# Kernel tuning notes

Measured on AMD Instinct MI355X. Metric: run time of the kernel, lower is better.

Reference implementation:

```python
import jax, jax.numpy as jnp
import numpy as np

B, T, C = 4, 2048, 1024
N_HEAD = 16
HEAD_DIM = C // N_HEAD


def setup_inputs() -> dict:
    key = jax.random.key(0)
    k1, k2, k3 = jax.random.split(key, 3)
    scale = 0.02
    x = jax.random.normal(k1, (B, T, C), dtype=jnp.float32)
    W_attn = jax.random.normal(k2, (C, 3 * C), dtype=jnp.float32) * scale
    b_attn = jnp.zeros((3 * C,), dtype=jnp.float32)
    W_proj = jax.random.normal(k3, (C, C), dtype=jnp.float32) * scale
    b_proj = jnp.zeros((C,), dtype=jnp.float32)
    return {"x": x, "W_attn": W_attn, "b_attn": b_attn, "W_proj": W_proj, "b_proj": b_proj}


def reference(x, W_attn, b_attn, W_proj, b_proj):
    Bx, Tx, Cx = x.shape
    qkv = x @ W_attn + b_attn                      # [B,T,3C]
    q, k, v = jnp.split(qkv, 3, axis=-1)
    def split_heads(t):
        return t.reshape(Bx, Tx, N_HEAD, HEAD_DIM).transpose(0, 2, 1, 3)  # [B,H,T,D]
    q, k, v = split_heads(q), split_heads(k), split_heads(v)
    att = jnp.einsum('bhqd,bhkd->bhqk', q, k) / jnp.sqrt(jnp.float32(HEAD_DIM))
    causal = jnp.tril(jnp.ones((Tx, Tx), dtype=bool))
    att = jnp.where(causal, att, jnp.float32(-jnp.inf))
    att = jax.nn.softmax(att, axis=-1)
    y = jnp.einsum('bhqk,bhkd->bhqd', att, v)      # [B,H,T,D]
    y = y.transpose(0, 2, 1, 3).reshape(Bx, Tx, Cx)
    return y @ W_proj + b_proj
```

## Files before the change

kernel.cpp:

```cpp
#include <hip/hip_runtime.h>
#include <hip/hip_bf16.h>
#include <math.h>

#define B_  4
#define T_  2048
#define C_  1024
#define NH  16
#define HD  64
#define M_  (B_ * T_)
#define N_QKV (3 * C_)
#define KDIM 1024
#define SCALE2 0.18033688011112042f

typedef __attribute__((ext_vector_type(8))) short short8;
typedef __attribute__((ext_vector_type(4))) short bs4;
typedef __attribute__((ext_vector_type(4))) float f32x4;
typedef __attribute__((ext_vector_type(16))) float f32x16;
typedef __attribute__((ext_vector_type(4))) unsigned u32x4;

__device__ __forceinline__ short f2bs(float f) {
  __hip_bfloat16 h = __float2bfloat16(f);
  return *reinterpret_cast<short*>(&h);
}
__device__ __forceinline__ unsigned pack2(float a, float b) {
  return (unsigned)(unsigned short)f2bs(a) | ((unsigned)(unsigned short)f2bs(b) << 16);
}

__device__ __forceinline__ void gload16(const void* g, void* l) {
  __builtin_amdgcn_global_load_lds(
      (const __attribute__((address_space(1))) void*)g,
      (__attribute__((address_space(3))) void*)l, 16, 0, 0);
}

__global__ __launch_bounds__(256) void wtrans_kernel(
    const float* __restrict__ W, short* __restrict__ Wt, int Ncols, int qcols)
{
  __shared__ short t[32][33];
  const int nb = Ncols / 32;
  const int bn = blockIdx.x % nb, bk = blockIdx.x / nb;
  const int tid = threadIdx.x;
  const int r = tid >> 3, c4 = (tid & 7) * 4;
  const float cs = (bn * 32 < qcols) ? SCALE2 : 1.f;
  f32x4 v = *reinterpret_cast<const f32x4*>(
      W + (size_t)(bk * 32 + r) * Ncols + bn * 32 + c4);
  #pragma unroll
  for (int j = 0; j < 4; ++j) t[r][c4 + j] = f2bs(v[j] * cs);
  __syncthreads();
  bs4 o;
  #pragma unroll
  for (int j = 0; j < 4; ++j) o[j] = t[c4 + j][r];
  *reinterpret_cast<bs4*>(Wt + (size_t)(bn * 32 + r) * KDIM + bk * 32 + c4) = o;
}

template<bool A_BF16, bool OUT_BF16>
__global__ __launch_bounds__(256) void gemm128_kernel(
    const void* __restrict__ Aptr, const short* __restrict__ Bt,
    const float* __restrict__ bias, void* __restrict__ outptr, int N, int nq)
{
  __shared__ short As[128 * 32];
  __shared__ short Bs[128 * 32];

  const int tid  = threadIdx.x;
  const int lane = tid & 63;
  const int w    = tid >> 6;
  const int wr   = w >> 1, wc = w & 1;
  const int rl   = lane & 15, kg = lane >> 4;
  const int nblk = N >> 7;
  const int m0 = (blockIdx.x / nblk) << 7;
  const int n0 = (blockIdx.x % nblk) << 7;

  f32x4 acc[4][4] = {};

  const int srow = w * 32 + (lane >> 2);
  const int scol = ((lane & 3) ^ ((lane >> 3) & 3)) * 8;
  const short* pb0 = Bt + (size_t)(n0 + srow) * KDIM + scol;
  const short* pb1 = pb0 + (size_t)16 * KDIM;
  short* const lb0 = &Bs[w * 1024];
  short* const lb1 = &Bs[w * 1024 + 512];

  const short* pa0 = nullptr; const short* pa1 = nullptr;
  short* la0 = nullptr; short* la1 = nullptr;
  const float* paf = nullptr; short* lafA = nullptr; short* lafB = nullptr;
  if constexpr (A_BF16) {
    pa0 = (const short*)Aptr + (size_t)(m0 + srow) * KDIM + scol;
    pa1 = pa0 + (size_t)16 * KDIM;
    la0 = &As[w * 1024];
    la1 = &As[w * 1024 + 512];
  } else {
    const int arow  = w * 32 + (lane >> 1);
    const int half  = lane & 1;
    const int phase = (lane >> 2) & 3;
    paf  = (const float*)Aptr + (size_t)(m0 + arow) * KDIM + half * 16;
    lafA = &As[arow * 32 + ((2 * half)     ^ phase) * 8];
    lafB = &As[arow * 32 + ((2 * half + 1) ^ phase) * 8];
  }

  const int sread = (kg ^ ((rl >> 1) & 3)) * 8;

  for (int k0 = 0; k0 < KDIM; k0 += 32) {
    __syncthreads();
    if constexpr (A_BF16) {
      gload16(pa0 + k0, la0);
      gload16(pa1 + k0, la1);
    } else {
      const float* p = paf + k0;
      f32x4 f0 = *reinterpret_cast<const f32x4*>(p);
      f32x4 f1 = *reinterpret_cast<const f32x4*>(p + 4);
      f32x4 f2 = *reinterpret_cast<const f32x4*>(p + 8);
      f32x4 f3 = *reinterpret_cast<const f32x4*>(p + 12);
      short8 lo, hi;
      #pragma unroll
      for (int j = 0; j < 4; ++j) {
        lo[j] = f2bs(f0[j]); lo[4 + j] = f2bs(f1[j]);
        hi[j] = f2bs(f2[j]); hi[4 + j] = f2bs(f3[j]);
      }
      *reinterpret_cast<short8*>(lafA) = lo;
      *reinterpret_cast<short8*>(lafB) = hi;
    }
    gload16(pb0 + k0, lb0);
    gload16(pb1 + k0, lb1);
    __syncthreads();

    short8 af[4], bf[4];
    #pragma unroll
    for (int i = 0; i < 4; ++i) {
      af[i] = *reinterpret_cast<short8*>(&As[(wr * 64 + i * 16 + rl) * 32 + sread]);
      bf[i] = *reinterpret_cast<short8*>(&Bs[(wc * 64 + i * 16 + rl) * 32 + sread]);
    }
    #pragma unroll
    for (int mi = 0; mi < 4; ++mi)
      #pragma unroll
      for (int ni = 0; ni < 4; ++ni)
        acc[mi][ni] = __builtin_amdgcn_mfma_f32_16x16x32_bf16(
            af[mi], bf[ni], acc[mi][ni], 0, 0, 0);
  }

  #pragma unroll
  for (int ni = 0; ni < 4; ++ni) {
    const int col = n0 + wc * 64 + ni * 16 + rl;
    float bv = bias[col];
    if (col < nq) bv *= SCALE2;
    #pragma unroll
    for (int mi = 0; mi < 4; ++mi) {
      #pragma unroll
      for (int r = 0; r < 4; ++r) {
        const int row = m0 + wr * 64 + mi * 16 + kg * 4 + r;
        const float v = acc[mi][ni][r] + bv;
        if constexpr (OUT_BF16)
          ((short*)outptr)[(size_t)row * N + col] = f2bs(v);
        else
          ((float*)outptr)[(size_t)row * N + col] = v;
      }
    }
  }
}

__global__ __launch_bounds__(256) void attn_mfma4_kernel(
    const short* __restrict__ qkv, short* __restrict__ y)
{
  __shared__ short Ks[2][64 * 64];
  __shared__ short Vt[2][64 * 64];

  const int tid  = threadIdx.x;
  const int lane = tid & 63;
  const int w    = tid >> 6;
  const int q32  = lane & 31;
  const int hi   = lane >> 5;

  const int bid  = blockIdx.x;
  const int qi   = 15 - (bid >> 6);
  const int bh   = bid & 63;
  const int b    = bh >> 4, h = bh & 15;
  const size_t bT = (size_t)b * T_;

  const int kr0 = tid >> 3;
  const int kl0 = (tid & 7) ^ ((tid >> 3) & 7);
  const int kr1 = (tid + 256) >> 3;
  const int kl1 = (tid & 7) ^ (((tid + 256) >> 3) & 7);
  const size_t kbase0 = (bT + kr0) * N_QKV + C_ + h * HD + kl0 * 8;
  const size_t kbase1 = (bT + kr1) * N_QKV + C_ + h * HD + kl1 * 8;
  short* const kdst0 = &Ks[0][(w * 64) * 8];
  short* const kdst1 = &Ks[0][(w * 64 + 256) * 8];

  const int vkey = tid & 63;
  const int vd16 = (tid >> 6) * 16;
  const size_t vbase = (bT + vkey) * N_QKV + 2 * C_ + h * HD + vd16;

  const int ksl = q32 & 7;

  const int nkb = 2 * qi + 2;
  const int wq0 = qi * 128 + w * 32;
  const int q   = wq0 + q32;

  short8 qf[4];
  #pragma unroll
  for (int kd = 0; kd < 4; ++kd)
    qf[kd] = *reinterpret_cast<const short8*>(
        qkv + (bT + q) * N_QKV + h * HD + kd * 16 + hi * 8);

  f32x16 o0 = {}, o1 = {};
  float m_ = -INFINITY, l_ = 0.f;

  {
    gload16(qkv + kbase0, kdst0);
    gload16(qkv + kbase1, kdst1);
    short8 va = *reinterpret_cast<const short8*>(qkv + vbase);
    short8 vb = *reinterpret_cast<const short8*>(qkv + vbase + 8);
    #pragma unroll
    for (int j = 0; j < 8; ++j) {
      Vt[0][(vd16 + j) * 64 + (((vkey >> 3) ^ j) << 3) + (vkey & 7)]     = va[j];
      Vt[0][(vd16 + 8 + j) * 64 + (((vkey >> 3) ^ j) << 3) + (vkey & 7)] = vb[j];
    }
  }
  __syncthreads();

  int cur = 0;
  for (int kb = 0; kb < nkb; ++kb) {
    const bool more = (kb + 1 < nkb);
    short8 va, vb;
    if (more) {
      const size_t koff = (size_t)(kb + 1) * 64 * N_QKV;
      gload16(qkv + kbase0 + koff, kdst0 + (cur ^ 1) * 4096);
      gload16(qkv + kbase1 + koff, kdst1 + (cur ^ 1) * 4096);
      va = *reinterpret_cast<const short8*>(qkv + vbase + koff);
      vb = *reinterpret_cast<const short8*>(qkv + vbase + koff + 8);
    }

    const int kmin = kb * 64;
    if (kmin <= wq0 + 31) {
      const short* ksc = &Ks[cur][0];
      const short* vtc = &Vt[cur][0];

      f32x16 s0 = {}, s1 = {};
      #pragma unroll
      for (int kd = 0; kd < 4; ++kd) {
        const int sl = ((2 * kd + hi) ^ ksl) * 8;
        short8 kf0 = *reinterpret_cast<const short8*>(&ksc[q32 * 64 + sl]);
        short8 kf1 = *reinterpret_cast<const short8*>(&ksc[(32 + q32) * 64 + sl]);
        s0 = __builtin_amdgcn_mfma_f32_32x32x16_bf16(kf0, qf[kd], s0, 0, 0, 0);
        s1 = __builtin_amdgcn_mfma_f32_32x32x16_bf16(kf1, qf[kd], s1, 0, 0, 0);
      }

      if (kmin + 63 > wq0) {
        const int qrel = q - kmin - 4 * hi;
        #pragma unroll
        for (int e = 0; e < 16; ++e) {
          const int ko = (e & 3) + 8 * (e >> 2);
          if (ko > qrel)      s0[e] = -INFINITY;
          if (ko + 32 > qrel) s1[e] = -INFINITY;
        }
      }

      float mx = s0[0];
      #pragma unroll
      for (int e = 1; e < 16; ++e) mx = fmaxf(mx, s0[e]);
      #pragma unroll
      for (int e = 0; e < 16; ++e) mx = fmaxf(mx, s1[e]);
      mx = fmaxf(mx, __shfl_xor(mx, 32, 64));

      if (!__all(mx <= m_ + 8.f)) {
        const float mn = fmaxf(m_, mx);
        const float cr = exp2f(m_ - mn);
        m_ = mn;
        l_ *= cr;
        #pragma unroll
        for (int e = 0; e < 16; ++e) { o0[e] *= cr; o1[e] *= cr; }
      }

      float rs = 0.f;
      #pragma unroll
      for (int e = 0; e < 16; ++e) {
        s0[e] = exp2f(s0[e] - m_); rs += s0[e];
        s1[e] = exp2f(s1[e] - m_); rs += s1[e];
      }
      rs += __shfl_xor(rs, 32, 64);
      l_ += rs;

      unsigned pk[2][4][2], sw[2][4][2];
      #pragma unroll
      for (int g = 0; g < 4; ++g)
        #pragma unroll
        for (int p = 0; p < 2; ++p) {
          pk[0][g][p] = pack2(s0[4 * g + 2 * p], s0[4 * g + 2 * p + 1]);
          pk[1][g][p] = pack2(s1[4 * g + 2 * p], s1[4 * g + 2 * p + 1]);
          sw[0][g][p] = (unsigned)__shfl_xor((int)pk[0][g][p], 32, 64);
          sw[1][g][p] = (unsigned)__shfl_xor((int)pk[1][g][p], 32, 64);
        }

      #pragma unroll
      for (int kk = 0; kk < 4; ++kk) {
        const int c = kk >> 1, a2 = 2 * (kk & 1);
        u32x4 t;
        t[0] = hi ? sw[c][a2 + 1][0] : pk[c][a2][0];
        t[1] = hi ? sw[c][a2 + 1][1] : pk[c][a2][1];
        t[2] = hi ? pk[c][a2 + 1][0] : sw[c][a2][0];
        t[3] = hi ? pk[c][a2 + 1][1] : sw[c][a2][1];
        const short8 pb = __builtin_bit_cast(short8, t);
        const int sl = ((2 * kk + hi) ^ ksl) * 8;
        short8 vf0 = *reinterpret_cast<const short8*>(&vtc[q32 * 64 + sl]);
        short8 vf1 = *reinterpret_cast<const short8*>(&vtc[(32 + q32) * 64 + sl]);
        o0 = __builtin_amdgcn_mfma_f32_32x32x16_bf16(vf0, pb, o0, 0, 0, 0);
        o1 = __builtin_amdgcn_mfma_f32_32x32x16_bf16(vf1, pb, o1, 0, 0, 0);
      }
    }

    if (more) {
      #pragma unroll
      for (int j = 0; j < 8; ++j) {
        Vt[cur ^ 1][(vd16 + j) * 64 + (((vkey >> 3) ^ j) << 3) + (vkey & 7)]     = va[j];
        Vt[cur ^ 1][(vd16 + 8 + j) * 64 + (((vkey >> 3) ^ j) << 3) + (vkey & 7)] = vb[j];
      }
    }
    __syncthreads();
    cur ^= 1;
  }

  const float inv = 1.f / l_;
  short* const yp = y + (bT + q) * C_ + h * HD;
  #pragma unroll
  for (int g = 0; g < 4; ++g) {
    bs4 ov0, ov1;
    #pragma unroll
    for (int t = 0; t < 4; ++t) {
      ov0[t] = f2bs(o0[4 * g + t] * inv);
      ov1[t] = f2bs(o1[4 * g + t] * inv);
    }
    *reinterpret_cast<bs4*>(yp + 8 * g + 4 * hi)      = ov0;
    *reinterpret_cast<bs4*>(yp + 32 + 8 * g + 4 * hi) = ov1;
  }
}

extern "C" void kernel_launch(void* const* d_in, const int* in_sizes, int n_in,
                              void* d_out, int out_size, void* d_ws, size_t ws_size,
                              hipStream_t stream) {
  const float* x  = (const float*)d_in[0];
  const float* Wa = (const float*)d_in[1];
  const float* ba = (const float*)d_in[2];
  const float* Wp = (const float*)d_in[3];
  const float* bp = (const float*)d_in[4];

  short* qkvb = (short*)d_ws;
  short* yb   = qkvb + (size_t)M_ * N_QKV;
  short* WaT  = yb + (size_t)M_ * C_;
  short* WpT  = WaT;

  wtrans_kernel<<<(KDIM / 32) * (N_QKV / 32), 256, 0, stream>>>(Wa, WaT, N_QKV, C_);
  gemm128_kernel<false, true><<<(M_ / 128) * (N_QKV / 128), 256, 0, stream>>>(
      x, WaT, ba, qkvb, N_QKV, C_);
  wtrans_kernel<<<(KDIM / 32) * (C_ / 32), 256, 0, stream>>>(Wp, WpT, C_, 0);
  attn_mfma4_kernel<<<16 * B_ * NH, 256, 0, stream>>>(qkvb, yb);
  gemm128_kernel<true, false><<<(M_ / 128) * (C_ / 128), 256, 0, stream>>>(
      yb, WpT, bp, d_out, C_, 0);
}
```

Measured before the change: 229.0 us.

## Interleave causal block order, pack V transpose stores, raise MFMA wave priority

Block-to-query-tile mapping is changed from strictly heaviest-first to an interleaved heavy/light order, to balance causal work across CUs. The V transpose into LDS now loads two adjacent key rows per thread and writes packed 32-bit pairs instead of 16 scalar short stores, cutting LDS store instructions. s_setprio is raised around the MFMA loops so matrix work is favoured over other waves. The interleaved order may reduce the tail-balancing benefit of heaviest-first scheduling.

```diff
diff --git a/kernel.cpp b/kernel.cpp
--- a/kernel.cpp
+++ b/kernel.cpp
@@ -155,7 +155,7 @@
   }
 }
 
-__global__ __launch_bounds__(256) void attn_mfma4_kernel(
+__global__ __launch_bounds__(256) void attn_mfma8_kernel(
     const short* __restrict__ qkv, short* __restrict__ y)
 {
   __shared__ short Ks[2][64 * 64];
@@ -168,7 +168,8 @@
   const int hi   = lane >> 5;
 
   const int bid  = blockIdx.x;
-  const int qi   = 15 - (bid >> 6);
+  const int g    = bid >> 6;
+  const int qi   = (g < 4) ? 15 - g : (g < 8) ? g - 4 : (g < 12) ? 19 - g : g - 8;
   const int bh   = bid & 63;
   const int b    = bh >> 4, h = bh & 15;
   const size_t bT = (size_t)b * T_;
@@ -182,9 +183,11 @@
   short* const kdst0 = &Ks[0][(w * 64) * 8];
   short* const kdst1 = &Ks[0][(w * 64 + 256) * 8];
 
-  const int vkey = tid & 63;
-  const int vd16 = (tid >> 6) * 16;
-  const size_t vbase = (bT + vkey) * N_QKV + 2 * C_ + h * HD + vd16;
+  const int kp = tid & 31;
+  const int d0 = (tid >> 5) * 8;
+  const size_t vbaseA = (bT + 2 * kp) * N_QKV + 2 * C_ + h * HD + d0;
+  const size_t vbaseB = vbaseA + N_QKV;
+  const int vws = ((kp >> 2) << 3) + ((kp & 3) << 1);
 
   const int ksl = q32 & 7;
 
@@ -204,12 +207,14 @@
   {
     gload16(qkv + kbase0, kdst0);
     gload16(qkv + kbase1, kdst1);
-    short8 va = *reinterpret_cast<const short8*>(qkv + vbase);
-    short8 vb = *reinterpret_cast<const short8*>(qkv + vbase + 8);
+    short8 va = *reinterpret_cast<const short8*>(qkv + vbaseA);
+    short8 vb = *reinterpret_cast<const short8*>(qkv + vbaseB);
     #pragma unroll
     for (int j = 0; j < 8; ++j) {
-      Vt[0][(vd16 + j) * 64 + (((vkey >> 3) ^ j) << 3) + (vkey & 7)]     = va[j];
-      Vt[0][(vd16 + 8 + j) * 64 + (((vkey >> 3) ^ j) << 3) + (vkey & 7)] = vb[j];
+      unsigned pw = (unsigned)(unsigned short)va[j] |
+                    ((unsigned)(unsigned short)vb[j] << 16);
+      *reinterpret_cast<unsigned*>(
+          &Vt[0][(d0 + j) * 64 + (vws ^ (j << 3))]) = pw;
     }
   }
   __syncthreads();
@@ -222,8 +227,8 @@
       const size_t koff = (size_t)(kb + 1) * 64 * N_QKV;
       gload16(qkv + kbase0 + koff, kdst0 + (cur ^ 1) * 4096);
       gload16(qkv + kbase1 + koff, kdst1 + (cur ^ 1) * 4096);
-      va = *reinterpret_cast<const short8*>(qkv + vbase + koff);
-      vb = *reinterpret_cast<const short8*>(qkv + vbase + koff + 8);
+      va = *reinterpret_cast<const short8*>(qkv + vbaseA + koff);
+      vb = *reinterpret_cast<const short8*>(qkv + vbaseB + koff);
     }
 
     const int kmin = kb * 64;
@@ -232,6 +237,7 @@
       const short* vtc = &Vt[cur][0];
 
       f32x16 s0 = {}, s1 = {};
+      __builtin_amdgcn_s_setprio(1);
       #pragma unroll
       for (int kd = 0; kd < 4; ++kd) {
         const int sl = ((2 * kd + hi) ^ ksl) * 8;
@@ -240,6 +246,7 @@
         s0 = __builtin_amdgcn_mfma_f32_32x32x16_bf16(kf0, qf[kd], s0, 0, 0, 0);
         s1 = __builtin_amdgcn_mfma_f32_32x32x16_bf16(kf1, qf[kd], s1, 0, 0, 0);
       }
+      __builtin_amdgcn_s_setprio(0);
 
       if (kmin + 63 > wq0) {
         const int qrel = q - kmin - 4 * hi;
@@ -278,15 +285,16 @@
 
       unsigned pk[2][4][2], sw[2][4][2];
       #pragma unroll
-      for (int g = 0; g < 4; ++g)
+      for (int gg = 0; gg < 4; ++gg)
         #pragma unroll
         for (int p = 0; p < 2; ++p) {
-          pk[0][g][p] = pack2(s0[4 * g + 2 * p], s0[4 * g + 2 * p + 1]);
-          pk[1][g][p] = pack2(s1[4 * g + 2 * p], s1[4 * g + 2 * p + 1]);
-          sw[0][g][p] = (unsigned)__shfl_xor((int)pk[0][g][p], 32, 64);
-          sw[1][g][p] = (unsigned)__shfl_xor((int)pk[1][g][p], 32, 64);
+          pk[0][gg][p] = pack2(s0[4 * gg + 2 * p], s0[4 * gg + 2 * p + 1]);
+          pk[1][gg][p] = pack2(s1[4 * gg + 2 * p], s1[4 * gg + 2 * p + 1]);
+          sw[0][gg][p] = (unsigned)__shfl_xor((int)pk[0][gg][p], 32, 64);
+          sw[1][gg][p] = (unsigned)__shfl_xor((int)pk[1][gg][p], 32, 64);
         }
 
+      __builtin_amdgcn_s_setprio(1);
       #pragma unroll
       for (int kk = 0; kk < 4; ++kk) {
         const int c = kk >> 1, a2 = 2 * (kk & 1);
@@ -302,13 +310,16 @@
         o0 = __builtin_amdgcn_mfma_f32_32x32x16_bf16(vf0, pb, o0, 0, 0, 0);
         o1 = __builtin_amdgcn_mfma_f32_32x32x16_bf16(vf1, pb, o1, 0, 0, 0);
       }
+      __builtin_amdgcn_s_setprio(0);
     }
 
     if (more) {
       #pragma unroll
       for (int j = 0; j < 8; ++j) {
-        Vt[cur ^ 1][(vd16 + j) * 64 + (((vkey >> 3) ^ j) << 3) + (vkey & 7)]     = va[j];
-        Vt[cur ^ 1][(vd16 + 8 + j) * 64 + (((vkey >> 3) ^ j) << 3) + (vkey & 7)] = vb[j];
+        unsigned pw = (unsigned)(unsigned short)va[j] |
+                      ((unsigned)(unsigned short)vb[j] << 16);
+        *reinterpret_cast<unsigned*>(
+            &Vt[cur ^ 1][(d0 + j) * 64 + (vws ^ (j << 3))]) = pw;
       }
     }
     __syncthreads();
@@ -318,15 +329,15 @@
   const float inv = 1.f / l_;
   short* const yp = y + (bT + q) * C_ + h * HD;
   #pragma unroll
-  for (int g = 0; g < 4; ++g) {
+  for (int gg = 0; gg < 4; ++gg) {
     bs4 ov0, ov1;
     #pragma unroll
     for (int t = 0; t < 4; ++t) {
-      ov0[t] = f2bs(o0[4 * g + t] * inv);
-      ov1[t] = f2bs(o1[4 * g + t] * inv);
-    }
-    *reinterpret_cast<bs4*>(yp + 8 * g + 4 * hi)      = ov0;
-    *reinterpret_cast<bs4*>(yp + 32 + 8 * g + 4 * hi) = ov1;
+      ov0[t] = f2bs(o0[4 * gg + t] * inv);
+      ov1[t] = f2bs(o1[4 * gg + t] * inv);
+    }
+    *reinterpret_cast<bs4*>(yp + 8 * gg + 4 * hi)      = ov0;
+    *reinterpret_cast<bs4*>(yp + 32 + 8 * gg + 4 * hi) = ov1;
   }
 }
 
@@ -348,7 +359,7 @@
   gemm128_kernel<false, true><<<(M_ / 128) * (N_QKV / 128), 256, 0, stream>>>(
       x, WaT, ba, qkvb, N_QKV, C_);
   wtrans_kernel<<<(KDIM / 32) * (C_ / 32), 256, 0, stream>>>(Wp, WpT, C_, 0);
-  attn_mfma4_kernel<<<16 * B_ * NH, 256, 0, stream>>>(qkvb, yb);
+  attn_mfma8_kernel<<<16 * B_ * NH, 256, 0, stream>>>(qkvb, yb);
   gemm128_kernel<true, false><<<(M_ / 128) * (C_ / 128), 256, 0, stream>>>(
       yb, WpT, bp, d_out, C_, 0);
 }
```

Result: slower. 244.0 us (+6.5%).
